# Optimization experiments

Hardware: AMD Instinct MI355X
Metric: run time of the kernel (lower is better)

Reference implementation:

```python
import jax, jax.numpy as jnp
import numpy as np

STRIDE = 1
PADDING = 1  # zeros padding mode

def setup_inputs() -> dict:
    key = jax.random.key(0)
    k1, k2, k3 = jax.random.split(key, 3)
    N, C_in, H, W = 32, 128, 56, 56
    C_out, kH, kW = 256, 3, 3
    x = jax.random.normal(k1, (N, C_in, H, W), dtype=jnp.float32)
    fan_in = C_in * kH * kW
    weight = jax.random.normal(k2, (C_out, C_in, kH, kW), dtype=jnp.float32) / np.sqrt(fan_in)
    bias = jax.random.normal(k3, (C_out,), dtype=jnp.float32) * 0.01
    return {"x": x, "weight": weight, "bias": bias}

def reference(x, weight, bias):
    # Same math as the im2col unfold + GEMM: a standard 2D cross-correlation
    # with zero padding. Expressed as the fused implicit-GEMM conv primitive.
    out = jax.lax.conv_general_dilated(
        x, weight,
        window_strides=(STRIDE, STRIDE),
        padding=[(PADDING, PADDING), (PADDING, PADDING)],
        dimension_numbers=("NCHW", "OIHW", "NCHW"),
    )
    # bias broadcast over (N, C_out, H_out, W_out)
    return out + bias[None, :, None, None]
```

## Files before the change

kernel.cpp:

```cpp
#include <hip/hip_runtime.h>


typedef __attribute__((ext_vector_type(8))) short short8;
typedef __attribute__((ext_vector_type(4))) float float4v;

constexpr int NB = 32, CI = 128, HH = 56, WW = 56, CO = 256;
constexpr int HWP = HH * WW;
constexpr int HP = 58, WP = 58;
constexpr size_t XTP_BYTES = (size_t)NB * HP * WP * CI * 2;
constexpr size_t WT_OFF    = XTP_BYTES;
constexpr size_t WT_BYTES  = (size_t)9 * CO * CI * 2;
constexpr size_t WS_NEED   = WT_OFF + WT_BYTES;

__device__ inline ushort f2bf(float v) {
    union { float f; uint u; } c; c.f = v;
    uint u = c.u;
    return (ushort)((u + 0x7fffu + ((u >> 16) & 1u)) >> 16);
}

__global__ __launch_bounds__(256) void xform_x(const float* __restrict__ x,
                                               ushort* __restrict__ xTp) {
    int b = blockIdx.x;
    int cit = b & 3;
    int hwt = (b >> 2) % 49;
    int n   = b / (4 * 49);
    int ci0 = cit * 32, hw0 = hwt * 64;
    __shared__ float t[32][65];
    int tx = threadIdx.x;
    int col = tx & 63, r4 = tx >> 6;
#pragma unroll
    for (int rr = 0; rr < 8; ++rr) {
        int row = rr * 4 + r4;
        t[row][col] = x[((size_t)n * CI + ci0 + row) * HWP + hw0 + col];
    }
    __syncthreads();
    int i = tx & 31, j0 = tx >> 5;
#pragma unroll
    for (int jj = 0; jj < 8; ++jj) {
        int j = jj * 8 + j0;
        int hw = hw0 + j;
        int h = hw / WW, w = hw % WW;
        xTp[(((size_t)n * HP + h + 1) * WP + (w + 1)) * CI + ci0 + i] = f2bf(t[i][j]);
    }
}

__global__ __launch_bounds__(256) void xform_border(ushort* __restrict__ xTp) {
    int u = blockIdx.x * 256 + threadIdx.x;
    int ci8 = u & 15;
    int r = u >> 4;
    int n = r / 228, bb = r % 228;
    int hp, wp;
    if (bb < 58)       { hp = 0;  wp = bb; }
    else if (bb < 116) { hp = 57; wp = bb - 58; }
    else { int c = bb - 116; hp = 1 + (c >> 1); wp = (c & 1) * 57; }
    short8 z = (short8)0;
    *reinterpret_cast<short8*>(xTp + (((size_t)n * HP + hp) * WP + wp) * CI + ci8 * 8) = z;
}

__global__ __launch_bounds__(256) void xform_w(const float* __restrict__ w,
                                               ushort* __restrict__ wT) {
    int o = blockIdx.x * 256 + threadIdx.x;
    int ci = o & 127;
    int co = (o >> 7) & 255;
    int tap = o >> 15;
    wT[o] = f2bf(w[((size_t)co * CI + ci) * 9 + tap]);
}

__global__ __launch_bounds__(256) void gemm_conv(
    const ushort* __restrict__ xTp, const ushort* __restrict__ wT,
    const float* __restrict__ bias, float* __restrict__ out)
{
    __shared__ ushort As[2][128 * 64];
    __shared__ ushort Bs[2][128 * 64];

    int b = blockIdx.x;
    int logical = (b & 7) * 196 + (b >> 3);
    const int mblk = logical >> 1;
    const int cblk = logical & 1;

    const int tid = threadIdx.x, lane = tid & 63, wv = tid >> 6;
    const int wco = wv >> 1, wm = wv & 1;
    const int s = (lane & 7) ^ ((lane >> 3) & 7);

    int aOff[4], bOff[4];
#pragma unroll
    for (int q = 0; q < 4; ++q) {
        int r = wv * 32 + q * 8 + (lane >> 3);
        aOff[q] = (cblk * 128 + r) * CI + s * 8;
        int m = mblk * 128 + r;
        int n = m / HWP, hw = m % HWP, h = hw / WW, w = hw % WW;
        bOff[q] = ((n * HP + h + 1) * WP + (w + 1)) * CI + s * 8;
    }

    float4v acc[4][4];
#pragma unroll
    for (int i = 0; i < 4; ++i)
#pragma unroll
        for (int j = 0; j < 4; ++j) acc[i][j] = (float4v)(0.0f);

    auto STAGE = [&](int slot, int t) {
        int tap = t >> 1, cb = (t & 1) * 64;
        int dh = tap / 3 - 1, dw = tap % 3 - 1;
        int ao = tap * CO * CI + cb;
        int bo = (dh * WP + dw) * CI + cb;
        ushort* asb = &As[slot][0];
        ushort* bsb = &Bs[slot][0];
#pragma unroll
        for (int q = 0; q < 4; ++q)
            __builtin_amdgcn_global_load_lds(
                (const __attribute__((address_space(1))) uint*)(wT + aOff[q] + ao),
                (__attribute__((address_space(3))) uint*)(asb + (wv * 32 + q * 8) * 64),
                16, 0, 0);
#pragma unroll
        for (int q = 0; q < 4; ++q)
            __builtin_amdgcn_global_load_lds(
                (const __attribute__((address_space(1))) uint*)(xTp + bOff[q] + bo),
                (__attribute__((address_space(3))) uint*)(bsb + (wv * 32 + q * 8) * 64),
                16, 0, 0);
    };

    auto COMPUTE = [&](int slot) {
        const ushort* asb = &As[slot][0];
        const ushort* bsb = &Bs[slot][0];
#pragma unroll
        for (int kk = 0; kk < 2; ++kk) {
            short8 a[4], bf[4];
#pragma unroll
            for (int f = 0; f < 4; ++f) {
                int row = wco * 64 + f * 16 + (lane & 15);
                int ch = (kk * 4 + (lane >> 4)) ^ (row & 7);
                a[f] = *(const short8*)(asb + row * 64 + ch * 8);
            }
#pragma unroll
            for (int f = 0; f < 4; ++f) {
                int row = wm * 64 + f * 16 + (lane & 15);
                int ch = (kk * 4 + (lane >> 4)) ^ (row & 7);
                bf[f] = *(const short8*)(bsb + row * 64 + ch * 8);
            }
#pragma unroll
            for (int i = 0; i < 4; ++i)
#pragma unroll
                for (int j = 0; j < 4; ++j)
                    acc[i][j] = __builtin_amdgcn_mfma_f32_16x16x32_bf16(
                        a[i], bf[j], acc[i][j], 0, 0, 0);
        }
    };

    STAGE(0, 0);
    __syncthreads();

#pragma unroll 1
    for (int t = 0; t < 16; t += 2) {
        STAGE(1, t + 1);
        COMPUTE(0);
        __syncthreads();
        STAGE(0, t + 2);
        COMPUTE(1);
        __syncthreads();
    }
    STAGE(1, 17);
    COMPUTE(0);
    __syncthreads();
    COMPUTE(1);

    const int co0 = cblk * 128 + wco * 64;
    const int m0  = mblk * 128 + wm * 64;
    float bv[4][4];
#pragma unroll
    for (int i = 0; i < 4; ++i)
#pragma unroll
        for (int r = 0; r < 4; ++r)
            bv[i][r] = bias[co0 + i * 16 + (lane >> 4) * 4 + r];
#pragma unroll
    for (int j = 0; j < 4; ++j) {
        int m = m0 + j * 16 + (lane & 15);
        int n = m / HWP, hw = m % HWP;
        float* obase = out + (size_t)n * CO * HWP + hw;
#pragma unroll
        for (int i = 0; i < 4; ++i) {
            int co = co0 + i * 16 + (lane >> 4) * 4;
#pragma unroll
            for (int r = 0; r < 4; ++r)
                obase[(size_t)(co + r) * HWP] = acc[i][j][r] + bv[i][r];
        }
    }
}

__global__ __launch_bounds__(256) void conv_k(
    const float* __restrict__ x, const float* __restrict__ wgt,
    const float* __restrict__ bias, float* __restrict__ out)
{
    int idx = blockIdx.x * 256 + threadIdx.x;
    int wg = idx % 14; int t = idx / 14;
    int ho = t % 56; t /= 56;
    int cog = t % 64; int n = t / 64;
    int w0 = wg * 4, co0 = cog * 4;
    float acc[4][4];
#pragma unroll
    for (int j = 0; j < 4; ++j) {
        float bj = bias[co0 + j];
#pragma unroll
        for (int p = 0; p < 4; ++p) acc[j][p] = bj;
    }
    const float* xn = x + (size_t)n * CI * HWP;
    for (int ci = 0; ci < CI; ++ci) {
        float xr[3][6];
#pragma unroll
        for (int kh = 0; kh < 3; ++kh) {
            int hi = ho + kh - 1;
            if (hi >= 0 && hi < HH) {
                const float* row = xn + ((size_t)ci * HH + hi) * WW;
                float4 c = *reinterpret_cast<const float4*>(row + w0);
                xr[kh][1] = c.x; xr[kh][2] = c.y; xr[kh][3] = c.z; xr[kh][4] = c.w;
                xr[kh][0] = (w0 > 0) ? row[w0 - 1] : 0.0f;
                xr[kh][5] = (w0 + 4 < WW) ? row[w0 + 4] : 0.0f;
            } else {
#pragma unroll
                for (int q = 0; q < 6; ++q) xr[kh][q] = 0.0f;
            }
        }
#pragma unroll
        for (int j = 0; j < 4; ++j) {
            const float* wp = wgt + ((size_t)(co0 + j) * CI + ci) * 9;
            float wvv[9];
#pragma unroll
            for (int q = 0; q < 9; ++q) wvv[q] = wp[q];
#pragma unroll
            for (int kh = 0; kh < 3; ++kh)
#pragma unroll
                for (int kw = 0; kw < 3; ++kw)
#pragma unroll
                    for (int p = 0; p < 4; ++p)
                        acc[j][p] = fmaf(xr[kh][p + kw], wvv[kh * 3 + kw], acc[j][p]);
        }
    }
#pragma unroll
    for (int j = 0; j < 4; ++j) {
        float4 v = make_float4(acc[j][0], acc[j][1], acc[j][2], acc[j][3]);
        *reinterpret_cast<float4*>(out + (((size_t)n * CO + co0 + j) * HH + ho) * WW + w0) = v;
    }
}

extern "C" void kernel_launch(void* const* d_in, const int* in_sizes, int n_in,
                              void* d_out, int out_size, void* d_ws, size_t ws_size,
                              hipStream_t stream) {
    const float* x = (const float*)d_in[0];
    const float* w = (const float*)d_in[1];
    const float* b = (const float*)d_in[2];
    float* out = (float*)d_out;

    if (ws_size < WS_NEED) {
        hipLaunchKernelGGL(conv_k, dim3(6272), dim3(256), 0, stream, x, w, b, out);
        return;
    }

    ushort* xTp = (ushort*)d_ws;
    ushort* wT  = (ushort*)((char*)d_ws + WT_OFF);

    hipLaunchKernelGGL(xform_x, dim3(32 * 49 * 4), dim3(256), 0, stream, x, xTp);
    hipLaunchKernelGGL(xform_border, dim3(456), dim3(256), 0, stream, xTp);
    hipLaunchKernelGGL(xform_w, dim3(9 * CO * CI / 256), dim3(256), 0, stream, w, wT);
    hipLaunchKernelGGL(gemm_conv, dim3(784 * 2), dim3(256), 0, stream,
                       xTp, wT, b, out);
}
```

Baseline: 102.4 us.

## Enlarge GEMM tile to 256x256 with 8 waves and K=32 stages

The conv GEMM goes from a 128x128 output tile with 4 waves to a 256 (all output channels) x 256 pixel tile with 8 waves per block. Each wave now computes 128x64, and the K loop becomes 36 steps of 32 channels with a reshaped LDS layout. The aim is to cut redundant global loads, since input pixels are no longer fetched twice (once per channel half), and to raise the MFMA-to-load ratio. It also adds an explicit vmcnt wait, raw barriers and setprio around the MFMAs. The costs are that the grid shrinks to 392 blocks, roughly 1.5 waves on 256 CUs, and the larger accumulator raises register pressure.

```diff
diff --git a/kernel.cpp b/kernel.cpp
--- a/kernel.cpp
+++ b/kernel.cpp
@@ -66,7 +66,7 @@
     wT[o] = f2bf(w[((size_t)co * CI + ci) * 9 + tap]);
 }
 
-__global__ __launch_bounds__(256) void gemm_conv(
+__global__ __launch_bounds__(512, 2) void gemm_conv(
     const ushort* __restrict__ xTp, const ushort* __restrict__ wT,
     const float* __restrict__ bias, float* __restrict__ out)
 {
@@ -74,114 +74,116 @@
     __shared__ ushort Bs[2][128 * 64];
 
     int b = blockIdx.x;
-    int logical = (b & 7) * 196 + (b >> 3);
-    const int mblk = logical >> 1;
-    const int cblk = logical & 1;
+    const int mblk = (b & 7) * 49 + (b >> 3);
 
     const int tid = threadIdx.x, lane = tid & 63, wv = tid >> 6;
-    const int wco = wv >> 1, wm = wv & 1;
+    const int wr = wv >> 2;
+    const int wc = wv & 3;
     const int s = (lane & 7) ^ ((lane >> 3) & 7);
 
-    int aOff[4], bOff[4];
-#pragma unroll
-    for (int q = 0; q < 4; ++q) {
-        int r = wv * 32 + q * 8 + (lane >> 3);
-        aOff[q] = (cblk * 128 + r) * CI + s * 8;
-        int m = mblk * 128 + r;
+    int aBase[2], bBase[2];
+#pragma unroll
+    for (int q = 0; q < 2; ++q) {
+        int r = wv * 16 + q * 8 + (lane >> 3);
+        int row2 = 2 * r + (s >> 2);
+        aBase[q] = row2 * CI + (s & 3) * 8;
+        int m = mblk * 256 + row2;
         int n = m / HWP, hw = m % HWP, h = hw / WW, w = hw % WW;
-        bOff[q] = ((n * HP + h + 1) * WP + (w + 1)) * CI + s * 8;
-    }
-
-    float4v acc[4][4];
-#pragma unroll
-    for (int i = 0; i < 4; ++i)
+        bBase[q] = ((n * HP + h + 1) * WP + (w + 1)) * CI + (s & 3) * 8;
+    }
+
+    float4v acc[8][4];
+#pragma unroll
+    for (int i = 0; i < 8; ++i)
 #pragma unroll
         for (int j = 0; j < 4; ++j) acc[i][j] = (float4v)(0.0f);
 
     auto STAGE = [&](int slot, int t) {
-        int tap = t >> 1, cb = (t & 1) * 64;
+        int tap = t >> 2, qk = t & 3;
         int dh = tap / 3 - 1, dw = tap % 3 - 1;
-        int ao = tap * CO * CI + cb;
-        int bo = (dh * WP + dw) * CI + cb;
+        int ao = tap * (CO * CI) + qk * 32;
+        int bo = (dh * WP + dw) * CI + qk * 32;
         ushort* asb = &As[slot][0];
         ushort* bsb = &Bs[slot][0];
 #pragma unroll
-        for (int q = 0; q < 4; ++q)
+        for (int q = 0; q < 2; ++q)
             __builtin_amdgcn_global_load_lds(
-                (const __attribute__((address_space(1))) uint*)(wT + aOff[q] + ao),
-                (__attribute__((address_space(3))) uint*)(asb + (wv * 32 + q * 8) * 64),
+                (const __attribute__((address_space(1))) uint*)(wT + aBase[q] + ao),
+                (__attribute__((address_space(3))) uint*)(asb + (wv * 16 + q * 8) * 64),
                 16, 0, 0);
 #pragma unroll
-        for (int q = 0; q < 4; ++q)
+        for (int q = 0; q < 2; ++q)
             __builtin_amdgcn_global_load_lds(
-                (const __attribute__((address_space(1))) uint*)(xTp + bOff[q] + bo),
-                (__attribute__((address_space(3))) uint*)(bsb + (wv * 32 + q * 8) * 64),
+                (const __attribute__((address_space(1))) uint*)(xTp + bBase[q] + bo),
+                (__attribute__((address_space(3))) uint*)(bsb + (wv * 16 + q * 8) * 64),
                 16, 0, 0);
     };
 
-    auto COMPUTE = [&](int slot) {
-        const ushort* asb = &As[slot][0];
-        const ushort* bsb = &Bs[slot][0];
-#pragma unroll
-        for (int kk = 0; kk < 2; ++kk) {
-            short8 a[4], bf[4];
-#pragma unroll
-            for (int f = 0; f < 4; ++f) {
-                int row = wco * 64 + f * 16 + (lane & 15);
-                int ch = (kk * 4 + (lane >> 4)) ^ (row & 7);
-                a[f] = *(const short8*)(asb + row * 64 + ch * 8);
-            }
-#pragma unroll
-            for (int f = 0; f < 4; ++f) {
-                int row = wm * 64 + f * 16 + (lane & 15);
-                int ch = (kk * 4 + (lane >> 4)) ^ (row & 7);
-                bf[f] = *(const short8*)(bsb + row * 64 + ch * 8);
-            }
-#pragma unroll
-            for (int i = 0; i < 4; ++i)
-#pragma unroll
-                for (int j = 0; j < 4; ++j)
-                    acc[i][j] = __builtin_amdgcn_mfma_f32_16x16x32_bf16(
-                        a[i], bf[j], acc[i][j], 0, 0, 0);
-        }
-    };
-
     STAGE(0, 0);
-    __syncthreads();
 
 #pragma unroll 1
-    for (int t = 0; t < 16; t += 2) {
-        STAGE(1, t + 1);
-        COMPUTE(0);
-        __syncthreads();
-        STAGE(0, t + 2);
-        COMPUTE(1);
-        __syncthreads();
-    }
-    STAGE(1, 17);
-    COMPUTE(0);
-    __syncthreads();
-    COMPUTE(1);
-
-    const int co0 = cblk * 128 + wco * 64;
-    const int m0  = mblk * 128 + wm * 64;
-    float bv[4][4];
-#pragma unroll
-    for (int i = 0; i < 4; ++i)
+    for (int t = 0; t < 36; ++t) {
+        const int sl = t & 1;
+        if (t < 35) {
+            STAGE(sl ^ 1, t + 1);
+            asm volatile("s_waitcnt vmcnt(4)" ::: "memory");
+        } else {
+            asm volatile("s_waitcnt vmcnt(0)" ::: "memory");
+        }
+        __builtin_amdgcn_s_barrier();
+        asm volatile("" ::: "memory");
+
+        const ushort* asb = &As[sl][0];
+        const ushort* bsb = &Bs[sl][0];
+        short8 a[8], bf[4];
+#pragma unroll
+        for (int f = 0; f < 8; ++f) {
+            int co = wr * 128 + f * 16 + (lane & 15);
+            int r = co >> 1;
+            int ch = (((co & 1) * 4 + (lane >> 4))) ^ (r & 7);
+            a[f] = *(const short8*)(asb + r * 64 + ch * 8);
+        }
+#pragma unroll
+        for (int g = 0; g < 4; ++g) {
+            int mr = wc * 64 + g * 16 + (lane & 15);
+            int r = mr >> 1;
+            int ch = (((mr & 1) * 4 + (lane >> 4))) ^ (r & 7);
+            bf[g] = *(const short8*)(bsb + r * 64 + ch * 8);
+        }
+
+        __builtin_amdgcn_s_setprio(1);
+#pragma unroll
+        for (int f = 0; f < 8; ++f)
+#pragma unroll
+            for (int g = 0; g < 4; ++g)
+                acc[f][g] = __builtin_amdgcn_mfma_f32_16x16x32_bf16(
+                    a[f], bf[g], acc[f][g], 0, 0, 0);
+        __builtin_amdgcn_s_setprio(0);
+
+        asm volatile("" ::: "memory");
+        __builtin_amdgcn_s_barrier();
+        asm volatile("" ::: "memory");
+    }
+
+    const int co0 = wr * 128;
+    const int m0  = mblk * 256 + wc * 64;
+    float bv[8][4];
+#pragma unroll
+    for (int f = 0; f < 8; ++f)
 #pragma unroll
         for (int r = 0; r < 4; ++r)
-            bv[i][r] = bias[co0 + i * 16 + (lane >> 4) * 4 + r];
-#pragma unroll
-    for (int j = 0; j < 4; ++j) {
-        int m = m0 + j * 16 + (lane & 15);
+            bv[f][r] = bias[co0 + f * 16 + (lane >> 4) * 4 + r];
+#pragma unroll
+    for (int g = 0; g < 4; ++g) {
+        int m = m0 + g * 16 + (lane & 15);
         int n = m / HWP, hw = m % HWP;
         float* obase = out + (size_t)n * CO * HWP + hw;
 #pragma unroll
-        for (int i = 0; i < 4; ++i) {
-            int co = co0 + i * 16 + (lane >> 4) * 4;
+        for (int f = 0; f < 8; ++f) {
+            int co = co0 + f * 16 + (lane >> 4) * 4;
 #pragma unroll
             for (int r = 0; r < 4; ++r)
-                obase[(size_t)(co + r) * HWP] = acc[i][j][r] + bv[i][r];
+                obase[(size_t)(co + r) * HWP] = acc[f][g][r] + bv[f][r];
         }
     }
 }
@@ -260,6 +262,6 @@
     hipLaunchKernelGGL(xform_x, dim3(32 * 49 * 4), dim3(256), 0, stream, x, xTp);
     hipLaunchKernelGGL(xform_border, dim3(456), dim3(256), 0, stream, xTp);
     hipLaunchKernelGGL(xform_w, dim3(9 * CO * CI / 256), dim3(256), 0, stream, w, wT);
-    hipLaunchKernelGGL(gemm_conv, dim3(784 * 2), dim3(256), 0, stream,
+    hipLaunchKernelGGL(gemm_conv, dim3(392), dim3(512), 0, stream,
                        xTp, wT, b, out);
 }
```

After: 114.3 us. 1.12x slower.
